# Optimization experiments

Measured on AMD Instinct MI355X. Metric: run time of the kernel, lower is better.

## Reference

```python
import jax, jax.numpy as jnp
import numpy as np

B, D, N0, N1 = 2, 512, 2048, 2048
ATT_DIM, OUT_DIM, H = 512, 512, 8
HEAD_ATT = ATT_DIM // H   # 64
HEAD_OUT = OUT_DIM // H   # 64
TEMP = 1.0
MASK_FILL = -10000000.0


def setup_inputs() -> dict:
    key = jax.random.key(0)
    ks = jax.random.split(key, 12)
    s = 0.02
    return {
        "feats_query": jax.random.normal(ks[0], (B, D, N0), dtype=jnp.float32),
        "feats_key": jax.random.normal(ks[1], (B, D, N1), dtype=jnp.float32),
        "key_mask": jax.random.randint(ks[2], (B, 1, N1), 0, 2, dtype=jnp.int32),
        # 1x1 Conv1d weights == (out_ch, in_ch) matrices
        "Wq": jax.random.normal(ks[3], (ATT_DIM, D), dtype=jnp.float32) * s,
        "bq": jnp.zeros((ATT_DIM,), dtype=jnp.float32),
        "Wk": jax.random.normal(ks[4], (ATT_DIM, D), dtype=jnp.float32) * s,
        "bk": jnp.zeros((ATT_DIM,), dtype=jnp.float32),
        "Wf": jax.random.normal(ks[5], (OUT_DIM, D), dtype=jnp.float32) * s,
        "bf": jnp.zeros((OUT_DIM,), dtype=jnp.float32),
        "Wm": jax.random.normal(ks[6], (OUT_DIM, OUT_DIM), dtype=jnp.float32) * s,
        "bm": jnp.zeros((OUT_DIM,), dtype=jnp.float32),
        "ln_g": jnp.ones((OUT_DIM,), dtype=jnp.float32),
        "ln_b": jnp.zeros((OUT_DIM,), dtype=jnp.float32),
    }


def _conv1x1(W, b, x):  # x: (b, in, n) -> (b, out, n)
    return jnp.einsum('oi,bin->bon', W, x) + b[None, :, None]


def reference(feats_query, feats_key, key_mask, Wq, bq, Wk, bk, Wf, bf, Wm, bm, ln_g, ln_b):
    b = feats_query.shape[0]
    n0 = feats_query.shape[2]
    n1 = feats_key.shape[2]
    # projections; channel split is (head_dim, head_num) per torch reshape
    q = _conv1x1(Wq, bq, feats_query).reshape(b, HEAD_ATT, H, n0)
    k = _conv1x1(Wk, bk, feats_key).reshape(b, HEAD_ATT, H, n1)
    v = _conv1x1(Wf, bf, feats_key).reshape(b, HEAD_OUT, H, n1)
    # attention: scores scaled by head_att_dim ** 0.5 (dim = query.shape[1])
    scores = jnp.einsum('bdhn,bdhm->bhnm', q / TEMP, k) / (HEAD_ATT ** 0.5)
    mask = key_mask.reshape(b, 1, 1, n1)
    scores = jnp.where(mask == 0, MASK_FILL, scores)
    prob = jax.nn.softmax(scores, axis=-1)
    feats_out = jnp.einsum('bhnm,bdhm->bdhn', prob, v).reshape(b, HEAD_OUT * H, n0)
    feats_out = _conv1x1(Wm, bm, feats_out)
    feats_out = feats_out + feats_query  # skip connection
    # SpecialLayerNorm: layernorm over channel dim (permute 0,2,1 -> LN -> permute back)
    x = feats_out.transpose(0, 2, 1)  # (b, n0, c)
    mu = jnp.mean(x, axis=-1, keepdims=True)
    var = jnp.var(x, axis=-1, keepdims=True)
    x = (x - mu) / jnp.sqrt(var + 1e-5) * ln_g + ln_b
    return x.transpose(0, 2, 1)  # (b, c, n0)
```

## Files before the change

### kernel.cpp

```cpp
#include <hip/hip_runtime.h>
#include <hip/hip_bf16.h>


using bf16x8 = __attribute__((ext_vector_type(8))) __bf16;
using f32x4  = __attribute__((ext_vector_type(4))) float;
using f32x16 = __attribute__((ext_vector_type(16))) float;
using us8    = __attribute__((ext_vector_type(8))) unsigned short;
using u32x4  = __attribute__((ext_vector_type(4))) unsigned int;

__device__ __forceinline__ unsigned short f2b(float f) {
  unsigned int u = __builtin_bit_cast(unsigned int, f);
  u += 0x7fffu + ((u >> 16) & 1u);
  return (unsigned short)(u >> 16);
}
__device__ __forceinline__ float b2f(unsigned short s) {
  unsigned int u = ((unsigned int)s) << 16;
  return __builtin_bit_cast(float, u);
}
__device__ __forceinline__ unsigned int cvtpk(float lo, float hi) {
  unsigned int w;
  asm("v_cvt_pk_bf16_f32 %0, %1, %2" : "=v"(w) : "v"(lo), "v"(hi));
  return w;
}
__device__ __forceinline__ void gl_lds16(const void* g, void* l) {
  __builtin_amdgcn_global_load_lds((const __attribute__((address_space(1))) void*)g,
                                   (__attribute__((address_space(3))) void*)l, 16, 0, 0);
}

__global__ __launch_bounds__(256) void k_pre(
    const float* __restrict__ fq, const float* __restrict__ fk,
    const float* __restrict__ Wq, const float* __restrict__ Wk,
    const float* __restrict__ Wf, const float* __restrict__ Wm,
    const int* __restrict__ mask,
    unsigned short* __restrict__ xqt, unsigned short* __restrict__ xkt,
    unsigned short* __restrict__ wqb, unsigned short* __restrict__ wkb,
    unsigned short* __restrict__ wfb, unsigned short* __restrict__ wmb,
    float* __restrict__ biasf)
{
  const int id = blockIdx.x;
  const int t = threadIdx.x;
  __shared__ float tile[64][65];

  if (id < 1024) {
    const int which = id >> 9;
    const int b = (id >> 8) & 1;
    const int i0 = ((id >> 5) & 7) * 64;
    const int n0 = (id & 31) * 64;
    const float* __restrict__ src = which ? fk : fq;
    unsigned short* __restrict__ dst = which ? xkt : xqt;
    const int cl = t & 63, rw = t >> 6;
    #pragma unroll
    for (int rr = 0; rr < 16; ++rr) {
      int il = rr * 4 + rw;
      tile[il][cl] = src[((size_t)b * 512 + i0 + il) * 2048 + n0 + cl];
    }
    __syncthreads();
    const int ci = (t & 31) * 2, rhalf = t >> 5;
    #pragma unroll
    for (int rr = 0; rr < 8; ++rr) {
      int nl = rr * 8 + rhalf;
      unsigned int v = (unsigned int)f2b(tile[ci][nl]) |
                       ((unsigned int)f2b(tile[ci + 1][nl]) << 16);
      *(unsigned int*)&dst[((size_t)b * 2048 + n0 + nl) * 512 + i0 + ci] = v;
    }
  } else if (id < 3072) {
    const int r = id - 1024;
    const int mat = r >> 9, cp = r & 511;
    if (mat < 3) {
      const float* W = (mat == 0) ? Wq : (mat == 1) ? Wk : Wf;
      unsigned short* O = (mat == 0) ? wqb : (mat == 1) ? wkb : wfb;
      const int orig = (cp & 63) * 8 + (cp >> 6);
      for (int j = t; j < 512; j += 256)
        O[cp * 512 + j] = f2b(W[orig * 512 + j]);
    } else {
      for (int j = t; j < 512; j += 256) {
        int h = j >> 6, d = j & 63;
        wmb[cp * 512 + j] = f2b(Wm[cp * 512 + d * 8 + h]);
      }
    }
  } else {
    const int r = id - 3072;
    if (r < 16) {
      int i = r * 256 + t;
      biasf[i] = mask[i] ? 0.f : -100000.f;
    }
  }
}

__global__ __launch_bounds__(256) void k_proj(
    const unsigned short* __restrict__ xqt, const unsigned short* __restrict__ xkt,
    const unsigned short* __restrict__ wqp, const unsigned short* __restrict__ wkp,
    const unsigned short* __restrict__ wfp,
    const float* __restrict__ bq, const float* __restrict__ bk, const float* __restrict__ bfv,
    unsigned short* __restrict__ Qb, unsigned short* __restrict__ Kb, unsigned short* __restrict__ VTb)
{
  const int lid = blockIdx.x;
  const int orig = (lid & 7) * 48 + (lid >> 3);
  const int z = orig >> 6;
  const int bid = orig & 63;
  const int b = z / 3, proj = z % 3;
  const int t = threadIdx.x, w = t >> 6, l = t & 63, q = l >> 4, m16 = l & 15;
  const int wm = w >> 1, wn = w & 1;

  __shared__ __attribute__((aligned(16))) unsigned short As[2][8192];
  __shared__ __attribute__((aligned(16))) unsigned short Bs[2][8192];

  const unsigned short* A;
  const unsigned short* Bt;
  int mt, nt_;
  if (proj < 2) {
    mt = bid >> 2; nt_ = bid & 3;
    A  = (proj == 0 ? xqt : xkt) + (size_t)b * 2048 * 512 + (size_t)mt * 128 * 512;
    Bt = (proj == 0 ? wqp : wkp) + (size_t)nt_ * 128 * 512;
  } else {
    mt = bid & 3; nt_ = bid >> 2;
    A  = wfp + (size_t)mt * 128 * 512;
    Bt = xkt + (size_t)b * 2048 * 512 + (size_t)nt_ * 128 * 512;
  }

  f32x4 acc[4][4];
  const f32x4 fz = {0.f, 0.f, 0.f, 0.f};
  #pragma unroll
  for (int mf = 0; mf < 4; ++mf)
    #pragma unroll
    for (int nf = 0; nf < 4; ++nf) acc[mf][nf] = fz;

#define PROJ_STAGE(BUF, KS)                                                          \
  {                                                                                  \
    _Pragma("unroll")                                                                \
    for (int c = 0; c < 4; ++c) {                                                    \
      int slot = c * 256 + t;                                                        \
      int row = slot >> 3, j = slot & 7;                                             \
      int jj = j ^ (row & 7);                                                        \
      gl_lds16(A  + (size_t)row * 512 + (KS) * 64 + jj * 8,                          \
               (char*)As[BUF] + (c * 256 + w * 64) * 16);                            \
      gl_lds16(Bt + (size_t)row * 512 + (KS) * 64 + jj * 8,                          \
               (char*)Bs[BUF] + (c * 256 + w * 64) * 16);                            \
    }                                                                                \
  }

  PROJ_STAGE(0, 0)
  asm volatile("s_waitcnt vmcnt(0)" ::: "memory");
  __syncthreads();

  for (int ks = 0; ks < 8; ++ks) {
    const int cur = ks & 1;
    if (ks < 7) PROJ_STAGE(cur ^ 1, ks + 1)
    #pragma unroll
    for (int kk = 0; kk < 2; ++kk) {
      bf16x8 av[4], bv[4];
      #pragma unroll
      for (int mf = 0; mf < 4; ++mf) {
        int row = wm * 64 + mf * 16 + m16;
        av[mf] = *(const bf16x8*)&As[cur][row * 64 + (((kk * 4 + q) ^ (row & 7)) << 3)];
      }
      #pragma unroll
      for (int nf = 0; nf < 4; ++nf) {
        int row = wn * 64 + nf * 16 + m16;
        bv[nf] = *(const bf16x8*)&Bs[cur][row * 64 + (((kk * 4 + q) ^ (row & 7)) << 3)];
      }
      #pragma unroll
      for (int mf = 0; mf < 4; ++mf)
        #pragma unroll
        for (int nf = 0; nf < 4; ++nf)
          acc[mf][nf] = __builtin_amdgcn_mfma_f32_16x16x32_bf16(av[mf], bv[nf], acc[mf][nf], 0, 0, 0);
    }
    if (ks < 7) {
      asm volatile("s_waitcnt vmcnt(0)" ::: "memory");
      __syncthreads();
    }
  }
#undef PROJ_STAGE

  const float QSCALE = 0.18033688011112042f;

  if (proj < 2) {
    const float* bias = (proj == 0) ? bq : bk;
    unsigned short* dst = (proj == 0) ? Qb : Kb;
    #pragma unroll
    for (int mf = 0; mf < 4; ++mf)
      #pragma unroll
      for (int nf = 0; nf < 4; ++nf)
        #pragma unroll
        for (int r = 0; r < 4; ++r) {
          int n  = mt * 128 + wm * 64 + mf * 16 + q * 4 + r;
          int cp = nt_ * 128 + wn * 64 + nf * 16 + m16;
          int h = cp >> 6, d = cp & 63;
          float v = acc[mf][nf][r] + bias[d * 8 + h];
          if (proj == 0) v *= QSCALE;
          dst[((size_t)(b * 8 + h) * 2048 + n) * 64 + d] = f2b(v);
        }
  } else {
    #pragma unroll
    for (int mf = 0; mf < 4; ++mf)
      #pragma unroll
      for (int nf = 0; nf < 4; ++nf)
        #pragma unroll
        for (int r = 0; r < 4; ++r) {
          int cp = mt * 128 + wm * 64 + mf * 16 + q * 4 + r;
          int n  = nt_ * 128 + wn * 64 + nf * 16 + m16;
          int h = cp >> 6, d = cp & 63;
          float v = acc[mf][nf][r] + bfv[d * 8 + h];
          VTb[((size_t)(b * 8 + h) * 64 + d) * 2048 + n] = f2b(v);
        }
  }
}

__global__ __launch_bounds__(256, 2) void k_attn2(
    const unsigned short* __restrict__ Qb, const unsigned short* __restrict__ Kb,
    const unsigned short* __restrict__ VTb, const float* __restrict__ biasf,
    unsigned short* __restrict__ OT)
{
  const int lid = blockIdx.x;
  const int orig = ((lid & 7) << 6) | (lid >> 3);
  const int bh = orig >> 5, b = bh >> 3, h = bh & 7;
  const int nt = orig & 31;
  const int t = threadIdx.x, w = t >> 6, l = t & 63;
  const int q31 = l & 31, hi = l >> 5;

  __shared__ __attribute__((aligned(16))) char lds_all[70656];
  char* kbuf = lds_all + w * 8192;
  char* vbuf = lds_all + 32768 + w * 8192;

  const unsigned short* Kp = Kb + (size_t)bh * (2048 * 64);
  const unsigned short* Vp = VTb + (size_t)bh * (64 * 2048);
  const float* brow = biasf + b * 2048;

  bf16x8 qfr[2][4];
  {
    const unsigned short* Qp = Qb + ((size_t)bh * 2048 + nt * 64) * 64;
    #pragma unroll
    for (int qf = 0; qf < 2; ++qf)
      #pragma unroll
      for (int tq = 0; tq < 4; ++tq)
        qfr[qf][tq] = *(const bf16x8*)&Qp[(qf * 32 + q31) * 64 + tq * 16 + hi * 8];
  }

  f32x16 z16;
  #pragma unroll
  for (int r = 0; r < 16; ++r) z16[r] = 0.f;

  f32x16 oacc[2][2];
  #pragma unroll
  for (int i = 0; i < 2; ++i)
    #pragma unroll
    for (int j2 = 0; j2 < 2; ++j2) oacc[i][j2] = z16;
  float lpart[2] = {0.f, 0.f};

  const int kr3 = l >> 3, ks3 = l & 7;
  const int vr4 = l >> 2, vs2 = l & 3;

  {
    int kv0 = w * 32;
    #pragma unroll
    for (int j = 0; j < 4; ++j)
      gl_lds16(Kp + (size_t)(kv0 + j * 8 + kr3) * 64 + (ks3 ^ kr3) * 8, kbuf + j * 1024);
    #pragma unroll
    for (int j = 0; j < 4; ++j) {
      int d = j * 16 + vr4;
      gl_lds16(Vp + (size_t)d * 2048 + kv0 + (vs2 ^ (d & 3)) * 8, vbuf + j * 1024);
    }
  }

  #pragma unroll 2
  for (int i = 0; i < 16; ++i) {
    const int bufi = i & 1;
    const int kv0 = (w + 4 * i) * 32;

    float4 bias[4];
    #pragma unroll
    for (int g = 0; g < 4; ++g)
      bias[g] = *(const float4*)&brow[kv0 + g * 8 + hi * 4];

    if (i < 15) {
      const int kvn = (w + 4 * (i + 1)) * 32;
      char* kb2 = kbuf + (bufi ^ 1) * 4096;
      char* vb2 = vbuf + (bufi ^ 1) * 4096;
      #pragma unroll
      for (int j = 0; j < 4; ++j)
        gl_lds16(Kp + (size_t)(kvn + j * 8 + kr3) * 64 + (ks3 ^ kr3) * 8, kb2 + j * 1024);
      #pragma unroll
      for (int j = 0; j < 4; ++j) {
        int d = j * 16 + vr4;
        gl_lds16(Vp + (size_t)d * 2048 + kvn + (vs2 ^ (d & 3)) * 8, vb2 + j * 1024);
      }
      asm volatile("s_waitcnt vmcnt(8)" ::: "memory");
    } else {
      asm volatile("s_waitcnt vmcnt(0)" ::: "memory");
    }
    __builtin_amdgcn_sched_barrier(0);

    const char* kb = kbuf + bufi * 4096;
    const char* vb = vbuf + bufi * 4096;

    bf16x8 ak[4];
    #pragma unroll
    for (int tq = 0; tq < 4; ++tq)
      ak[tq] = *(const bf16x8*)(kb + q31 * 128 + ((((tq << 1) | hi) ^ (q31 & 7)) * 16));

    f32x16 sacc[2];
    __builtin_amdgcn_s_setprio(1);
    sacc[0] = __builtin_amdgcn_mfma_f32_32x32x16_bf16(ak[0], qfr[0][0], z16, 0, 0, 0);
    sacc[1] = __builtin_amdgcn_mfma_f32_32x32x16_bf16(ak[0], qfr[1][0], z16, 0, 0, 0);
    #pragma unroll
    for (int tq = 1; tq < 4; ++tq) {
      sacc[0] = __builtin_amdgcn_mfma_f32_32x32x16_bf16(ak[tq], qfr[0][tq], sacc[0], 0, 0, 0);
      sacc[1] = __builtin_amdgcn_mfma_f32_32x32x16_bf16(ak[tq], qfr[1][tq], sacc[1], 0, 0, 0);
    }
    __builtin_amdgcn_s_setprio(0);

    bf16x8 av[2][2];
    #pragma unroll
    for (int df = 0; df < 2; ++df)
      #pragma unroll
      for (int tt = 0; tt < 2; ++tt)
        av[df][tt] = *(const bf16x8*)(vb + (df * 32 + q31) * 64 + ((((tt << 1) | hi) ^ (q31 & 3)) * 16));

    #pragma unroll
    for (int qf = 0; qf < 2; ++qf) {
      float e[16];
      #pragma unroll
      for (int g = 0; g < 4; ++g) {
        e[g*4+0] = __builtin_amdgcn_exp2f(sacc[qf][g*4+0] + bias[g].x);
        e[g*4+1] = __builtin_amdgcn_exp2f(sacc[qf][g*4+1] + bias[g].y);
        e[g*4+2] = __builtin_amdgcn_exp2f(sacc[qf][g*4+2] + bias[g].z);
        e[g*4+3] = __builtin_amdgcn_exp2f(sacc[qf][g*4+3] + bias[g].w);
      }
      float s0 = 0.f;
      #pragma unroll
      for (int r = 0; r < 16; ++r) s0 += e[r];
      lpart[qf] += s0;

      unsigned int W[8];
      #pragma unroll
      for (int j = 0; j < 8; ++j) W[j] = cvtpk(e[2*j], e[2*j+1]);
      asm("v_permlane32_swap_b32 %0, %1" : "+v"(W[0]), "+v"(W[2]));
      asm("v_permlane32_swap_b32 %0, %1" : "+v"(W[1]), "+v"(W[3]));
      asm("v_permlane32_swap_b32 %0, %1" : "+v"(W[4]), "+v"(W[6]));
      asm("v_permlane32_swap_b32 %0, %1" : "+v"(W[5]), "+v"(W[7]));
      u32x4 lo4 = {W[0], W[1], W[2], W[3]};
      u32x4 hi4 = {W[4], W[5], W[6], W[7]};
      bf16x8 pb0 = __builtin_bit_cast(bf16x8, lo4);
      bf16x8 pb1 = __builtin_bit_cast(bf16x8, hi4);

      __builtin_amdgcn_s_setprio(1);
      oacc[0][qf] = __builtin_amdgcn_mfma_f32_32x32x16_bf16(av[0][0], pb0, oacc[0][qf], 0, 0, 0);
      oacc[0][qf] = __builtin_amdgcn_mfma_f32_32x32x16_bf16(av[0][1], pb1, oacc[0][qf], 0, 0, 0);
      oacc[1][qf] = __builtin_amdgcn_mfma_f32_32x32x16_bf16(av[1][0], pb0, oacc[1][qf], 0, 0, 0);
      oacc[1][qf] = __builtin_amdgcn_mfma_f32_32x32x16_bf16(av[1][1], pb1, oacc[1][qf], 0, 0, 0);
      __builtin_amdgcn_s_setprio(0);
    }
  }

  float* pc = (float*)lds_all;
  float* ls = (float*)(lds_all + 69632);
  __syncthreads();
  #pragma unroll
  for (int qf = 0; qf < 2; ++qf) {
    float lfull = lpart[qf] + __shfl_xor(lpart[qf], 32);
    int qq = qf * 32 + q31;
    if (hi == 0) ls[w * 64 + qq] = lfull;
    #pragma unroll
    for (int df = 0; df < 2; ++df)
      #pragma unroll
      for (int g = 0; g < 4; ++g) {
        f32x4 v4 = {oacc[df][qf][g*4+0], oacc[df][qf][g*4+1],
                    oacc[df][qf][g*4+2], oacc[df][qf][g*4+3]};
        *(f32x4*)&pc[w * 4352 + qq * 68 + df * 32 + g * 8 + hi * 4] = v4;
      }
  }
  __syncthreads();
  {
    const int q = t >> 2, ds = (t & 3) * 16;
    float lsumv = ls[q] + ls[64 + q] + ls[128 + q] + ls[192 + q];
    f32x4 o4[4];
    #pragma unroll
    for (int j = 0; j < 4; ++j) o4[j] = *(const f32x4*)&pc[q * 68 + ds + j * 4];
    #pragma unroll
    for (int ww = 1; ww < 4; ++ww)
      #pragma unroll
      for (int j = 0; j < 4; ++j) {
        f32x4 p4 = *(const f32x4*)&pc[ww * 4352 + q * 68 + ds + j * 4];
        o4[j] += p4;
      }
    float rinv = __builtin_amdgcn_rcpf(lsumv);
    unsigned int pk[8];
    #pragma unroll
    for (int j = 0; j < 4; ++j) {
      pk[2*j]   = cvtpk(o4[j][0] * rinv, o4[j][1] * rinv);
      pk[2*j+1] = cvtpk(o4[j][2] * rinv, o4[j][3] * rinv);
    }
    unsigned short* dst = &OT[((size_t)b * 2048 + nt * 64 + q) * 512 + h * 64 + ds];
    u32x4 s0 = {pk[0], pk[1], pk[2], pk[3]};
    u32x4 s1 = {pk[4], pk[5], pk[6], pk[7]};
    *(u32x4*)dst = s0;
    *(u32x4*)(dst + 8) = s1;
  }
}

__global__ __launch_bounds__(256) void k_out(
    const unsigned short* __restrict__ OT, const unsigned short* __restrict__ wmw,
    const float* __restrict__ bm, const float* __restrict__ fq,
    const float* __restrict__ g, const float* __restrict__ be,
    float* __restrict__ out)
{
  const int b = blockIdx.y;
  const int n0 = blockIdx.x * 32;
  const int t = threadIdx.x, w = t >> 6, l = t & 63, q = l >> 4, m16 = l & 15;

  __shared__ __attribute__((aligned(16))) unsigned short As[2][2048];
  __shared__ __attribute__((aligned(16))) unsigned short Bs[2][32768];
  __shared__ float ssum[4][32], ssq[4][32];

  f32x4 acc[2][8];
  const f32x4 fz = {0.f, 0.f, 0.f, 0.f};
  #pragma unroll
  for (int mf = 0; mf < 2; ++mf)
    #pragma unroll
    for (int nf = 0; nf < 8; ++nf) acc[mf][nf] = fz;

  const unsigned short* Abase = OT + ((size_t)b * 2048 + n0) * 512;
  const unsigned short* Bbase = wmw;

#define OUT_STAGE(BUF, KS)                                                          \
  {                                                                                 \
    { int row = t >> 3, j = t & 7;                                                  \
      gl_lds16(Abase + (size_t)row * 512 + (KS) * 64 + ((j ^ (row & 7)) * 8),       \
               (char*)As[BUF] + w * 1024); }                                        \
    _Pragma("unroll")                                                               \
    for (int c = 0; c < 16; ++c) {                                                  \
      int slot = c * 256 + t;                                                       \
      int row = slot >> 3, j = slot & 7;                                            \
      gl_lds16(Bbase + (size_t)row * 512 + (KS) * 64 + ((j ^ (row & 7)) * 8),       \
               (char*)Bs[BUF] + (c * 256 + w * 64) * 16);                           \
    }                                                                               \
  }

  OUT_STAGE(0, 0)
  asm volatile("s_waitcnt vmcnt(0)" ::: "memory");
  __syncthreads();

  for (int ks = 0; ks < 8; ++ks) {
    const int cur = ks & 1;
    if (ks < 7) OUT_STAGE(cur ^ 1, ks + 1)
    #pragma unroll
    for (int kk = 0; kk < 2; ++kk) {
      bf16x8 av[2];
      #pragma unroll
      for (int mf = 0; mf < 2; ++mf) {
        int row = mf * 16 + m16;
        av[mf] = *(const bf16x8*)((const char*)As[cur] + row * 128 + (((kk * 4 + q) ^ (row & 7)) * 16));
      }
      #pragma unroll
      for (int nf = 0; nf < 8; ++nf) {
        int row = w * 128 + nf * 16 + m16;
        bf16x8 bv = *(const bf16x8*)((const char*)Bs[cur] + row * 128 + (((kk * 4 + q) ^ (row & 7)) * 16));
        acc[0][nf] = __builtin_amdgcn_mfma_f32_16x16x32_bf16(av[0], bv, acc[0][nf], 0, 0, 0);
        acc[1][nf] = __builtin_amdgcn_mfma_f32_16x16x32_bf16(av[1], bv, acc[1][nf], 0, 0, 0);
      }
    }
    if (ks < 7) {
      asm volatile("s_waitcnt vmcnt(0)" ::: "memory");
      __syncthreads();
    }
  }
#undef OUT_STAGE

  float gv[8], bev[8], bmv[8];
  #pragma unroll
  for (int nf = 0; nf < 8; ++nf) {
    int c = w * 128 + nf * 16 + m16;
    gv[nf] = g[c]; bev[nf] = be[c]; bmv[nf] = bm[c];
  }
  #pragma unroll
  for (int mf = 0; mf < 2; ++mf)
    #pragma unroll
    for (int nf = 0; nf < 8; ++nf) {
      int c = w * 128 + nf * 16 + m16;
      f32x4 res = *(const f32x4*)&fq[((size_t)b * 512 + c) * 2048 + n0 + mf * 16 + q * 4];
      #pragma unroll
      for (int r = 0; r < 4; ++r)
        acc[mf][nf][r] += bmv[nf] + res[r];
    }
  #pragma unroll
  for (int mf = 0; mf < 2; ++mf)
    #pragma unroll
    for (int r = 0; r < 4; ++r) {
      float ps = 0.f, pss = 0.f;
      #pragma unroll
      for (int nf = 0; nf < 8; ++nf) {
        float v = acc[mf][nf][r];
        ps += v; pss += v * v;
      }
      ps += __shfl_xor(ps, 1); pss += __shfl_xor(pss, 1);
      ps += __shfl_xor(ps, 2); pss += __shfl_xor(pss, 2);
      ps += __shfl_xor(ps, 4); pss += __shfl_xor(pss, 4);
      ps += __shfl_xor(ps, 8); pss += __shfl_xor(pss, 8);
      if (m16 == 0) {
        ssum[w][mf * 16 + q * 4 + r] = ps;
        ssq[w][mf * 16 + q * 4 + r] = pss;
      }
    }
  __syncthreads();
  #pragma unroll
  for (int mf = 0; mf < 2; ++mf)
    #pragma unroll
    for (int r = 0; r < 4; ++r) {
      int nl = mf * 16 + q * 4 + r;
      float S  = ssum[0][nl] + ssum[1][nl] + ssum[2][nl] + ssum[3][nl];
      float SS = ssq[0][nl] + ssq[1][nl] + ssq[2][nl] + ssq[3][nl];
      float mu = S * (1.f / 512.f);
      float var = SS * (1.f / 512.f) - mu * mu;
      float rstd = rsqrtf(var + 1e-5f);
      #pragma unroll
      for (int nf = 0; nf < 8; ++nf)
        acc[mf][nf][r] = (acc[mf][nf][r] - mu) * rstd * gv[nf] + bev[nf];
    }
  #pragma unroll
  for (int mf = 0; mf < 2; ++mf)
    #pragma unroll
    for (int nf = 0; nf < 8; ++nf) {
      int c = w * 128 + nf * 16 + m16;
      *(f32x4*)&out[((size_t)b * 512 + c) * 2048 + n0 + mf * 16 + q * 4] = acc[mf][nf];
    }
}

extern "C" void kernel_launch(void* const* d_in, const int* in_sizes, int n_in,
                              void* d_out, int out_size, void* d_ws, size_t ws_size,
                              hipStream_t stream) {
  const float* fq  = (const float*)d_in[0];
  const float* fk  = (const float*)d_in[1];
  const int*   msk = (const int*)d_in[2];
  const float* Wq  = (const float*)d_in[3];
  const float* bq  = (const float*)d_in[4];
  const float* Wk  = (const float*)d_in[5];
  const float* bk  = (const float*)d_in[6];
  const float* Wf  = (const float*)d_in[7];
  const float* bfv = (const float*)d_in[8];
  const float* Wm  = (const float*)d_in[9];
  const float* bm  = (const float*)d_in[10];
  const float* lng = (const float*)d_in[11];
  const float* lnb = (const float*)d_in[12];
  float* out = (float*)d_out;

  char* ws = (char*)d_ws;
  const size_t MB = 1024 * 1024;
  unsigned short* xqt = (unsigned short*)(ws + 0 * MB);
  unsigned short* xkt = (unsigned short*)(ws + 4 * MB);
  unsigned short* wqb = (unsigned short*)(ws + 8 * MB);
  unsigned short* wkb = (unsigned short*)(ws + 8 * MB + 512 * 1024);
  unsigned short* wfb = (unsigned short*)(ws + 9 * MB);
  unsigned short* wmb = (unsigned short*)(ws + 9 * MB + 512 * 1024);
  unsigned short* Qb  = (unsigned short*)(ws + 10 * MB);
  unsigned short* Kb  = (unsigned short*)(ws + 14 * MB);
  unsigned short* VTb = (unsigned short*)(ws + 18 * MB);
  unsigned short* OTb = (unsigned short*)(ws + 22 * MB);
  float*          biasf = (float*)(ws + 26 * MB);

  hipLaunchKernelGGL(k_pre, dim3(3088), dim3(256), 0, stream,
                     fq, fk, Wq, Wk, Wf, Wm, msk, xqt, xkt, wqb, wkb, wfb, wmb, biasf);
  hipLaunchKernelGGL(k_proj, dim3(384), dim3(256), 0, stream,
                     xqt, xkt, wqb, wkb, wfb, bq, bk, bfv, Qb, Kb, VTb);
  hipLaunchKernelGGL(k_attn2, dim3(512), dim3(256), 0, stream, Qb, Kb, VTb, biasf, OTb);
  hipLaunchKernelGGL(k_out, dim3(64, 2), dim3(256), 0, stream,
                     OTb, wmb, bm, fq, lng, lnb, out);
}
```

Before: 72.99 us.

## Load K/V fragments directly into registers with register double-buffering instead of LDS

The attention kernel stops staging K and V tiles through LDS with async global-to-LDS copies and waitcnt-managed double buffering. Each wave now loads its MFMA operand fragments straight from global memory into registers, ping-ponging between two register sets so the next tile's loads overlap the current tile's compute. The QK^T MFMAs are also interleaved per query fragment, and a sync before the epilogue is dropped. This removes LDS round trips and the waitcnt stalls, but raises register pressure and relies on the compiler to schedule the global loads early. The direct global reads are less coalesced, especially the strided V^T rows.

New measurement: 83.91 us. 15.0% more time.

```diff
diff --git a/kernel.cpp b/kernel.cpp
--- a/kernel.cpp
+++ b/kernel.cpp
@@ -206,7 +206,7 @@
   }
 }
 
-__global__ __launch_bounds__(256, 2) void k_attn2(
+__global__ __launch_bounds__(256, 2) void k_attn4(
     const unsigned short* __restrict__ Qb, const unsigned short* __restrict__ Kb,
     const unsigned short* __restrict__ VTb, const float* __restrict__ biasf,
     unsigned short* __restrict__ OT)
@@ -219,8 +219,6 @@
   const int q31 = l & 31, hi = l >> 5;
 
   __shared__ __attribute__((aligned(16))) char lds_all[70656];
-  char* kbuf = lds_all + w * 8192;
-  char* vbuf = lds_all + 32768 + w * 8192;
 
   const unsigned short* Kp = Kb + (size_t)bh * (2048 * 64);
   const unsigned short* Vp = VTb + (size_t)bh * (64 * 2048);
@@ -239,97 +237,53 @@
   f32x16 z16;
   #pragma unroll
   for (int r = 0; r < 16; ++r) z16[r] = 0.f;
-
   f32x16 oacc[2][2];
-  #pragma unroll
-  for (int i = 0; i < 2; ++i)
-    #pragma unroll
-    for (int j2 = 0; j2 < 2; ++j2) oacc[i][j2] = z16;
+  oacc[0][0] = z16; oacc[0][1] = z16; oacc[1][0] = z16; oacc[1][1] = z16;
   float lpart[2] = {0.f, 0.f};
 
-  const int kr3 = l >> 3, ks3 = l & 7;
-  const int vr4 = l >> 2, vs2 = l & 3;
-
-  {
-    int kv0 = w * 32;
-    #pragma unroll
-    for (int j = 0; j < 4; ++j)
-      gl_lds16(Kp + (size_t)(kv0 + j * 8 + kr3) * 64 + (ks3 ^ kr3) * 8, kbuf + j * 1024);
-    #pragma unroll
-    for (int j = 0; j < 4; ++j) {
-      int d = j * 16 + vr4;
-      gl_lds16(Vp + (size_t)d * 2048 + kv0 + (vs2 ^ (d & 3)) * 8, vbuf + j * 1024);
-    }
-  }
-
-  #pragma unroll 2
-  for (int i = 0; i < 16; ++i) {
-    const int bufi = i & 1;
+  auto LK = [&](int i, bf16x8 (&kk)[4], bf16x8 (&vv)[4]) {
     const int kv0 = (w + 4 * i) * 32;
-
+    #pragma unroll
+    for (int tq = 0; tq < 4; ++tq)
+      kk[tq] = *(const bf16x8*)&Kp[(size_t)(kv0 + q31) * 64 + tq * 16 + hi * 8];
+    #pragma unroll
+    for (int df = 0; df < 2; ++df)
+      #pragma unroll
+      for (int tt = 0; tt < 2; ++tt)
+        vv[df * 2 + tt] = *(const bf16x8*)&Vp[(size_t)(df * 32 + q31) * 2048 + kv0 + tt * 16 + hi * 8];
+  };
+
+  auto COMPUTE = [&](int i, bf16x8 (&kk)[4], bf16x8 (&vv)[4]) {
+    const int kv0 = (w + 4 * i) * 32;
     float4 bias[4];
     #pragma unroll
     for (int g = 0; g < 4; ++g)
       bias[g] = *(const float4*)&brow[kv0 + g * 8 + hi * 4];
 
-    if (i < 15) {
-      const int kvn = (w + 4 * (i + 1)) * 32;
-      char* kb2 = kbuf + (bufi ^ 1) * 4096;
-      char* vb2 = vbuf + (bufi ^ 1) * 4096;
-      #pragma unroll
-      for (int j = 0; j < 4; ++j)
-        gl_lds16(Kp + (size_t)(kvn + j * 8 + kr3) * 64 + (ks3 ^ kr3) * 8, kb2 + j * 1024);
-      #pragma unroll
-      for (int j = 0; j < 4; ++j) {
-        int d = j * 16 + vr4;
-        gl_lds16(Vp + (size_t)d * 2048 + kvn + (vs2 ^ (d & 3)) * 8, vb2 + j * 1024);
-      }
-      asm volatile("s_waitcnt vmcnt(8)" ::: "memory");
-    } else {
-      asm volatile("s_waitcnt vmcnt(0)" ::: "memory");
-    }
-    __builtin_amdgcn_sched_barrier(0);
-
-    const char* kb = kbuf + bufi * 4096;
-    const char* vb = vbuf + bufi * 4096;
-
-    bf16x8 ak[4];
-    #pragma unroll
-    for (int tq = 0; tq < 4; ++tq)
-      ak[tq] = *(const bf16x8*)(kb + q31 * 128 + ((((tq << 1) | hi) ^ (q31 & 7)) * 16));
-
-    f32x16 sacc[2];
-    __builtin_amdgcn_s_setprio(1);
-    sacc[0] = __builtin_amdgcn_mfma_f32_32x32x16_bf16(ak[0], qfr[0][0], z16, 0, 0, 0);
-    sacc[1] = __builtin_amdgcn_mfma_f32_32x32x16_bf16(ak[0], qfr[1][0], z16, 0, 0, 0);
-    #pragma unroll
-    for (int tq = 1; tq < 4; ++tq) {
-      sacc[0] = __builtin_amdgcn_mfma_f32_32x32x16_bf16(ak[tq], qfr[0][tq], sacc[0], 0, 0, 0);
-      sacc[1] = __builtin_amdgcn_mfma_f32_32x32x16_bf16(ak[tq], qfr[1][tq], sacc[1], 0, 0, 0);
-    }
-    __builtin_amdgcn_s_setprio(0);
-
-    bf16x8 av[2][2];
-    #pragma unroll
-    for (int df = 0; df < 2; ++df)
-      #pragma unroll
-      for (int tt = 0; tt < 2; ++tt)
-        av[df][tt] = *(const bf16x8*)(vb + (df * 32 + q31) * 64 + ((((tt << 1) | hi) ^ (q31 & 3)) * 16));
-
     #pragma unroll
     for (int qf = 0; qf < 2; ++qf) {
+      f32x16 sacc;
+      __builtin_amdgcn_s_setprio(1);
+      sacc = __builtin_amdgcn_mfma_f32_32x32x16_bf16(kk[0], qfr[qf][0], z16, 0, 0, 0);
+      #pragma unroll
+      for (int tq = 1; tq < 4; ++tq)
+        sacc = __builtin_amdgcn_mfma_f32_32x32x16_bf16(kk[tq], qfr[qf][tq], sacc, 0, 0, 0);
+      __builtin_amdgcn_s_setprio(0);
+
       float e[16];
       #pragma unroll
       for (int g = 0; g < 4; ++g) {
-        e[g*4+0] = __builtin_amdgcn_exp2f(sacc[qf][g*4+0] + bias[g].x);
-        e[g*4+1] = __builtin_amdgcn_exp2f(sacc[qf][g*4+1] + bias[g].y);
-        e[g*4+2] = __builtin_amdgcn_exp2f(sacc[qf][g*4+2] + bias[g].z);
-        e[g*4+3] = __builtin_amdgcn_exp2f(sacc[qf][g*4+3] + bias[g].w);
-      }
-      float s0 = 0.f;
-      #pragma unroll
-      for (int r = 0; r < 16; ++r) s0 += e[r];
-      lpart[qf] += s0;
+        e[g*4+0] = __builtin_amdgcn_exp2f(sacc[g*4+0] + bias[g].x);
+        e[g*4+1] = __builtin_amdgcn_exp2f(sacc[g*4+1] + bias[g].y);
+        e[g*4+2] = __builtin_amdgcn_exp2f(sacc[g*4+2] + bias[g].z);
+        e[g*4+3] = __builtin_amdgcn_exp2f(sacc[g*4+3] + bias[g].w);
+      }
+      {
+        float s0 = e[0]+e[1], s1 = e[2]+e[3], s2 = e[4]+e[5], s3 = e[6]+e[7];
+        float s4 = e[8]+e[9], s5 = e[10]+e[11], s6 = e[12]+e[13], s7 = e[14]+e[15];
+        float t0 = s0+s1, t1 = s2+s3, t2 = s4+s5, t3 = s6+s7;
+        lpart[qf] += (t0+t1) + (t2+t3);
+      }
 
       unsigned int W[8];
       #pragma unroll
@@ -344,17 +298,25 @@
       bf16x8 pb1 = __builtin_bit_cast(bf16x8, hi4);
 
       __builtin_amdgcn_s_setprio(1);
-      oacc[0][qf] = __builtin_amdgcn_mfma_f32_32x32x16_bf16(av[0][0], pb0, oacc[0][qf], 0, 0, 0);
-      oacc[0][qf] = __builtin_amdgcn_mfma_f32_32x32x16_bf16(av[0][1], pb1, oacc[0][qf], 0, 0, 0);
-      oacc[1][qf] = __builtin_amdgcn_mfma_f32_32x32x16_bf16(av[1][0], pb0, oacc[1][qf], 0, 0, 0);
-      oacc[1][qf] = __builtin_amdgcn_mfma_f32_32x32x16_bf16(av[1][1], pb1, oacc[1][qf], 0, 0, 0);
+      oacc[0][qf] = __builtin_amdgcn_mfma_f32_32x32x16_bf16(vv[0], pb0, oacc[0][qf], 0, 0, 0);
+      oacc[0][qf] = __builtin_amdgcn_mfma_f32_32x32x16_bf16(vv[1], pb1, oacc[0][qf], 0, 0, 0);
+      oacc[1][qf] = __builtin_amdgcn_mfma_f32_32x32x16_bf16(vv[2], pb0, oacc[1][qf], 0, 0, 0);
+      oacc[1][qf] = __builtin_amdgcn_mfma_f32_32x32x16_bf16(vv[3], pb1, oacc[1][qf], 0, 0, 0);
       __builtin_amdgcn_s_setprio(0);
     }
+  };
+
+  bf16x8 kA[4], vA[4], kB[4], vB[4];
+  LK(0, kA, vA);
+  for (int ii = 0; ii < 8; ++ii) {
+    LK(2 * ii + 1, kB, vB);
+    COMPUTE(2 * ii, kA, vA);
+    if (ii < 7) LK(2 * ii + 2, kA, vA);
+    COMPUTE(2 * ii + 1, kB, vB);
   }
 
   float* pc = (float*)lds_all;
   float* ls = (float*)(lds_all + 69632);
-  __syncthreads();
   #pragma unroll
   for (int qf = 0; qf < 2; ++qf) {
     float lfull = lpart[qf] + __shfl_xor(lpart[qf], 32);
@@ -561,7 +523,7 @@
                      fq, fk, Wq, Wk, Wf, Wm, msk, xqt, xkt, wqb, wkb, wfb, wmb, biasf);
   hipLaunchKernelGGL(k_proj, dim3(384), dim3(256), 0, stream,
                      xqt, xkt, wqb, wkb, wfb, bq, bk, bfv, Qb, Kb, VTb);
-  hipLaunchKernelGGL(k_attn2, dim3(512), dim3(256), 0, stream, Qb, Kb, VTb, biasf, OTb);
+  hipLaunchKernelGGL(k_attn4, dim3(512), dim3(256), 0, stream, Qb, Kb, VTb, biasf, OTb);
   hipLaunchKernelGGL(k_out, dim3(64, 2), dim3(256), 0, stream,
                      OTb, wmb, bm, fq, lng, lnb, out);
 }
```
